# Optimization experiments

Hardware: AMD Instinct MI355X
Metric: run time of the kernel (lower is better)

The kernel has to match this reference:

```python
import jax, jax.numpy as jnp
import numpy as np

B, N, D = 4, 2048, 1024

def setup_inputs() -> dict:
    key = jax.random.key(0)
    ks = jax.random.split(key, 8)
    s = 1.0 / np.sqrt(D)
    return {
        "x": jax.random.normal(ks[0], (B, N, D), dtype=jnp.float32),
        "Wq": jax.random.normal(ks[1], (D, D), dtype=jnp.float32) * s,
        "bq": jnp.zeros((D,), dtype=jnp.float32),
        "Wk": jax.random.normal(ks[2], (D, D), dtype=jnp.float32) * s,
        "bk": jnp.zeros((D,), dtype=jnp.float32),
        "Wv": jax.random.normal(ks[3], (D, D), dtype=jnp.float32) * s,
        "bv": jnp.zeros((D,), dtype=jnp.float32),
        "gamma": jnp.ones((1,), dtype=jnp.float32),
    }

def reference(x, Wq, bq, Wk, bk, Wv, bv, gamma):
    d = x.shape[-1]
    delta = 1.0 / jnp.sqrt(jnp.asarray(d, dtype=x.dtype))
    # torch Linear: y = x @ W.T + b, W is [out, in]
    Q = jnp.einsum('bnd,ed->bne', x, Wq) + bq
    K = jnp.einsum('bnd,ed->bne', x, Wk) + bk
    V = jnp.einsum('bnd,ed->bne', x, Wv) + bv
    scores = jnp.einsum('bne,bme->bnm', Q, K) * delta  # [B, N, N]
    attn = jax.nn.softmax(scores, axis=-1)
    out = jnp.einsum('bnm,bme->bne', attn, V)
    return out * gamma + x
```

## Files before the change

kernel.cpp:

```cpp
#include <hip/hip_runtime.h>

typedef _Float16 f16;
typedef __attribute__((ext_vector_type(4))) _Float16 f16x4;
typedef __attribute__((ext_vector_type(8))) _Float16 f16x8;
typedef __attribute__((ext_vector_type(4))) float f32x4;

#define B_ 4
#define N_ 2048
#define D_ 1024

#define FENCE asm volatile("" ::: "memory")

__global__ __launch_bounds__(256) void k_cast_all(const float4* __restrict__ x,
                                                  const float4* __restrict__ wq,
                                                  const float4* __restrict__ wk,
                                                  const float4* __restrict__ wv,
                                                  f16x4* __restrict__ xo,
                                                  f16x4* __restrict__ wqo,
                                                  f16x4* __restrict__ wko,
                                                  f16x4* __restrict__ wvo,
                                                  float* __restrict__ rowsum) {
  int b = blockIdx.x;
  if (b >= 11264) {
    rowsum[(b - 11264) * 256 + threadIdx.x] = 0.f;
    return;
  }
  const float4* in;
  f16x4* out;
  int idx;
  if (b < 8192)       { in = x;  out = xo;  idx = b * 256 + threadIdx.x; }
  else if (b < 9216)  { in = wq; out = wqo; idx = (b - 8192) * 256 + threadIdx.x; }
  else if (b < 10240) { in = wk; out = wko; idx = (b - 9216) * 256 + threadIdx.x; }
  else                { in = wv; out = wvo; idx = (b - 10240) * 256 + threadIdx.x; }
  float4 v = in[idx];
  f16x4 o = { (_Float16)v.x, (_Float16)v.y, (_Float16)v.z, (_Float16)v.w };
  out[idx] = o;
}

__device__ __forceinline__ void stage_half(const char* g0, int ldB, int kByte,
                                           char* slot, int tid) {
#pragma unroll
  for (int r = 0; r < 2; ++r) {
    int lin = r * 8192 + tid * 16;
    int row = lin >> 7;
    int lch = ((lin >> 4) & 7) ^ (row & 7);
    const char* g = g0 + (long)row * ldB + kByte + lch * 16;
    char* l = slot + r * 8192 + ((tid >> 6) << 10);
    __builtin_amdgcn_global_load_lds(
        (const __attribute__((address_space(1))) unsigned int*)g,
        (__attribute__((address_space(3))) unsigned int*)l, 16, 0, 0);
  }
}

#define RD_A(dst, base)                                                          \
  _Pragma("unroll") for (int i_ = 0; i_ < 4; ++i_) {                             \
    int rA_ = wm * 64 + i_ * 16 + l16;                                           \
    _Pragma("unroll") for (int k_ = 0; k_ < 2; ++k_)                             \
      dst[i_][k_] = *(const f16x8*)((base) + rA_ * 128 +                         \
                                    ((((k_ << 2) | quad) ^ l7) << 4));           \
  }
#define RD_B(dst, base)                                                          \
  _Pragma("unroll") for (int j_ = 0; j_ < 2; ++j_) {                             \
    int rB_ = wn * 32 + j_ * 16 + l16;                                           \
    _Pragma("unroll") for (int k_ = 0; k_ < 2; ++k_)                             \
      dst[j_][k_] = *(const f16x8*)((base) + rB_ * 128 +                         \
                                    ((((k_ << 2) | quad) ^ l7) << 4));           \
  }
#define MFMA8(Av, Bv, BH)                                                        \
  __builtin_amdgcn_s_setprio(1);                                                 \
  _Pragma("unroll") for (int i_ = 0; i_ < 4; ++i_)                               \
  _Pragma("unroll") for (int j_ = 0; j_ < 2; ++j_)                               \
  _Pragma("unroll") for (int k_ = 0; k_ < 2; ++k_)                               \
    acc[i_][BH][j_] = __builtin_amdgcn_mfma_f32_16x16x32_f16(                    \
        Av[i_][k_], Bv[j_][k_], acc[i_][BH][j_], 0, 0, 0);                       \
  __builtin_amdgcn_s_setprio(0);
#define MFMA16(Av, Bv, AH, BH)                                                   \
  __builtin_amdgcn_s_setprio(1);                                                 \
  _Pragma("unroll") for (int i_ = 0; i_ < 4; ++i_)                               \
  _Pragma("unroll") for (int j_ = 0; j_ < 2; ++j_)                               \
  _Pragma("unroll") for (int k_ = 0; k_ < 2; ++k_)                               \
    acc[AH][i_][BH][j_] = __builtin_amdgcn_mfma_f32_16x16x32_f16(                \
        Av[i_][k_], Bv[j_][k_], acc[AH][i_][BH][j_], 0, 0, 0);                   \
  __builtin_amdgcn_s_setprio(0);

__device__ __forceinline__ void gemm256(const char* gA, int ldaB,
                                        const char* gB, int ldbB,
                                        int nK, char* lds, f32x4 acc[2][4][2][2]) {
  const int tid = threadIdx.x;
  const int lane = tid & 63, wave = tid >> 6;
  const int wm = wave >> 2, wn = wave & 3;
  const int quad = lane >> 4, l16 = lane & 15;
  const int l7 = l16 & 7;
  const char* gA1 = gA + (long)128 * ldaB;
  const char* gB1 = gB + (long)128 * ldbB;
  char* Abuf = lds;
  char* Bbuf = lds + 65536;
  f16x8 a0[4][2], a1[4][2], bX[2][2], bY[2][2];
  stage_half(gA,  ldaB, 0, Abuf, tid);
  stage_half(gB,  ldbB, 0, Bbuf, tid);
  stage_half(gA1, ldaB, 0, Abuf + 16384, tid);
  stage_half(gB1, ldbB, 0, Bbuf + 16384, tid);
  asm volatile("s_waitcnt vmcnt(4)" ::: "memory");
  __builtin_amdgcn_s_barrier(); FENCE;
  RD_A(a0, Abuf); RD_B(bX, Bbuf);
  for (int t = 0; t < nK; ++t) {
    const int c = t & 1;
    char* Ac = Abuf + c * 32768;
    char* Bc = Bbuf + c * 32768;
    char* An = Abuf + (c ^ 1) * 32768;
    char* Bn = Bbuf + (c ^ 1) * 32768;
    const bool st = (t + 1 < nK);
    const int kB = (t + 1) << 7;
    if (st) { stage_half(gA, ldaB, kB, An, tid); stage_half(gB, ldbB, kB, Bn, tid); }
    if (st) asm volatile("s_waitcnt vmcnt(6)" ::: "memory");
    else    asm volatile("s_waitcnt vmcnt(2)" ::: "memory");
    __builtin_amdgcn_s_barrier(); FENCE;
    RD_A(a1, Ac + 16384);
    MFMA16(a0, bX, 0, 0);
    if (st) asm volatile("s_waitcnt vmcnt(4)" ::: "memory");
    else    asm volatile("s_waitcnt vmcnt(0)" ::: "memory");
    __builtin_amdgcn_s_barrier(); FENCE;
    RD_B(bY, Bc + 16384);
    MFMA16(a1, bX, 1, 0);
    if (st) { stage_half(gA1, ldaB, kB, An + 16384, tid); stage_half(gB1, ldbB, kB, Bn + 16384, tid); }
    if (st) asm volatile("s_waitcnt vmcnt(4)" ::: "memory");
    __builtin_amdgcn_s_barrier(); FENCE;
    if (st) RD_B(bX, Bn);
    MFMA16(a0, bY, 0, 1);
    __builtin_amdgcn_s_barrier(); FENCE;
    if (st) RD_A(a0, An);
    MFMA16(a1, bY, 1, 1);
  }
  asm volatile("s_waitcnt vmcnt(0)" ::: "memory");
  __builtin_amdgcn_s_barrier();
  FENCE;
}

#define D128_TILE(AC, B0C, AN, B0N, q) {                                         \
  char* Sc = lds + (q) * 49152;                                                  \
  char* Sn = lds + ((q) ^ 1) * 49152;                                            \
  const int kB = (t + 1) << 7;                                                   \
  stage_half(gA, ldaB, kB, Sn, tid);                                             \
  stage_half(gB, ldbB, kB, Sn + 16384, tid);                                     \
  asm volatile("s_waitcnt vmcnt(4)" ::: "memory");                               \
  __builtin_amdgcn_s_barrier(); FENCE;                                           \
  RD_B(b1, Sc + 32768);                                                          \
  MFMA8(AC, B0C, 0);                                                             \
  stage_half(gB1, ldbB, kB, Sn + 32768, tid);                                    \
  asm volatile("s_waitcnt vmcnt(2)" ::: "memory");                               \
  __builtin_amdgcn_s_barrier(); FENCE;                                           \
  RD_A(AN, Sn); RD_B(B0N, Sn + 16384);                                           \
  MFMA8(AC, b1, 1);                                                              \
}
#define D128_TAIL(AC, B0C, q) {                                                  \
  char* Sc = lds + (q) * 49152;                                                  \
  asm volatile("s_waitcnt vmcnt(0)" ::: "memory");                               \
  __builtin_amdgcn_s_barrier(); FENCE;                                           \
  RD_B(b1, Sc + 32768);                                                          \
  MFMA8(AC, B0C, 0);                                                             \
  MFMA8(AC, b1, 1);                                                              \
}

__device__ __forceinline__ void gemm_d128(const char* gA, int ldaB,
                                          const char* gB, int ldbB,
                                          int nK, char* lds, f32x4 acc[4][2][2]) {
  const int tid = threadIdx.x;
  const int lane = tid & 63, wave = tid >> 6;
  const int wm = wave >> 2, wn = wave & 3;
  const int quad = lane >> 4, l16 = lane & 15;
  const int l7 = l16 & 7;
  const char* gB1 = gB + (long)128 * ldbB;
  f16x8 aX[4][2], aY[4][2], b0X[2][2], b0Y[2][2], b1[2][2];
  stage_half(gA,  ldaB, 0, lds, tid);
  stage_half(gB,  ldbB, 0, lds + 16384, tid);
  stage_half(gB1, ldbB, 0, lds + 32768, tid);
  asm volatile("s_waitcnt vmcnt(2)" ::: "memory");
  __builtin_amdgcn_s_barrier(); FENCE;
  RD_A(aX, lds); RD_B(b0X, lds + 16384);
  for (int tb = 0; tb < nK - 2; tb += 2) {
    { const int t = tb;     D128_TILE(aX, b0X, aY, b0Y, 0) }
    { const int t = tb + 1; D128_TILE(aY, b0Y, aX, b0X, 1) }
  }
  { const int t = nK - 2;   D128_TILE(aX, b0X, aY, b0Y, 0) }
  D128_TAIL(aY, b0Y, 1)
  __builtin_amdgcn_s_barrier(); FENCE;
}

__global__ __launch_bounds__(512, 2) void k_qkv(const f16* __restrict__ X,
                                                const f16* __restrict__ Wq,
                                                const f16* __restrict__ Wk,
                                                const f16* __restrict__ Wv,
                                                const float* __restrict__ bq,
                                                const float* __restrict__ bk,
                                                const float* __restrict__ bv,
                                                f16* __restrict__ Q, f16* __restrict__ Ko,
                                                f16* __restrict__ Vt) {
  __shared__ __align__(16) char lds[131072];
  int fid = blockIdx.x;
  int xcd = fid & 7, k = fid >> 3;
  int rowt = xcd * 4 + (k & 3);
  int colt = k >> 2;
  int tm = rowt * 256;
  int w = colt >> 2;
  int tn = (colt & 3) * 256;
  const f16* Wsel = (w == 0) ? Wq : (w == 1) ? Wk : Wv;
  f32x4 acc[2][4][2][2];
#pragma unroll
  for (int Ah = 0; Ah < 2; ++Ah)
#pragma unroll
    for (int i = 0; i < 4; ++i)
#pragma unroll
      for (int Bh = 0; Bh < 2; ++Bh)
#pragma unroll
        for (int jn = 0; jn < 2; ++jn) acc[Ah][i][Bh][jn] = (f32x4){0.f, 0.f, 0.f, 0.f};
  gemm256((const char*)(X + (long)tm * D_), D_ * 2,
          (const char*)(Wsel + (long)tn * D_), D_ * 2, D_ / 64, lds, acc);
  const int tid = threadIdx.x;
  const int lane = tid & 63, wave = tid >> 6;
  const int wm = wave >> 2, wn = wave & 3;
  const int quad = lane >> 4, l16 = lane & 15;
  if (w < 2) {
    const float* bias = w ? bk : bq;
    f16* outp = w ? Ko : Q;
#pragma unroll
    for (int Bh = 0; Bh < 2; ++Bh)
#pragma unroll
      for (int jn = 0; jn < 2; ++jn) {
        int col = tn + Bh * 128 + wn * 32 + jn * 16 + l16;
        float bb = bias[col];
#pragma unroll
        for (int Ah = 0; Ah < 2; ++Ah)
#pragma unroll
          for (int i = 0; i < 4; ++i) {
            int rbase = tm + Ah * 128 + wm * 64 + i * 16 + quad * 4;
#pragma unroll
            for (int r = 0; r < 4; ++r)
              outp[(long)(rbase + r) * D_ + col] = (_Float16)(acc[Ah][i][Bh][jn][r] + bb);
          }
      }
  } else {
    int bidx = tm >> 11, ntok = tm & 2047;
    f16* VtB = Vt + (long)bidx * D_ * N_ + ntok;
    f16* ldsT = (f16*)lds;
#pragma unroll
    for (int pass = 0; pass < 2; ++pass) {
      FENCE;
      __builtin_amdgcn_s_barrier();
      FENCE;
#pragma unroll
      for (int jn = 0; jn < 2; ++jn) {
        int fl = wn * 32 + jn * 16 + l16;
        float bb = bv[tn + pass * 128 + fl];
#pragma unroll
        for (int Ah = 0; Ah < 2; ++Ah)
#pragma unroll
          for (int i = 0; i < 4; ++i) {
            int rl = Ah * 128 + wm * 64 + i * 16 + quad * 4;
            f16x4 p = { (_Float16)(acc[Ah][i][pass][jn][0] + bb),
                        (_Float16)(acc[Ah][i][pass][jn][1] + bb),
                        (_Float16)(acc[Ah][i][pass][jn][2] + bb),
                        (_Float16)(acc[Ah][i][pass][jn][3] + bb) };
            *(f16x4*)(ldsT + fl * 264 + rl) = p;
          }
      }
      FENCE;
      __builtin_amdgcn_s_barrier();
      FENCE;
#pragma unroll
      for (int p = 0; p < 8; ++p) {
        int f = p * 16 + (tid >> 5);
        int cc = tid & 31;
        f16x8 v = *(const f16x8*)(ldsT + f * 264 + cc * 8);
        *(f16x8*)(VtB + (long)(tn + pass * 128 + f) * N_ + cc * 8) = v;
      }
    }
  }
}

__global__ __launch_bounds__(512, 2) void k_scores(const f16* __restrict__ Qf,
                                                   const f16* __restrict__ Kf,
                                                   f16* __restrict__ S,
                                                   float* __restrict__ rowsum) {
  __shared__ __align__(16) char lds[131072];
  int fid = blockIdx.x;
  int xcd = fid & 7, k = fid >> 3;
  int lin = xcd * 32 + k;
  int b = lin >> 6;
  int t = lin & 63;
  int rowt = t & 7, colt = t >> 3;
  int tm = rowt * 256, tn = colt * 256;
  f32x4 acc[2][4][2][2];
#pragma unroll
  for (int Ah = 0; Ah < 2; ++Ah)
#pragma unroll
    for (int i = 0; i < 4; ++i)
#pragma unroll
      for (int Bh = 0; Bh < 2; ++Bh)
#pragma unroll
        for (int jn = 0; jn < 2; ++jn) acc[Ah][i][Bh][jn] = (f32x4){0.f, 0.f, 0.f, 0.f};
  gemm256((const char*)(Qf + (long)b * N_ * D_ + (long)tm * D_), D_ * 2,
          (const char*)(Kf + (long)b * N_ * D_ + (long)tn * D_), D_ * 2,
          D_ / 64, lds, acc);
  const int tid = threadIdx.x;
  const int lane = tid & 63, wave = tid >> 6;
  const int wm = wave >> 2, wn = wave & 3;
  const int quad = lane >> 4, l16 = lane & 15;
  f16* Sb = S + (long)b * N_ * N_;
  const float delta = 0.03125f;
  f16* ldsS = (f16*)lds;
  float rsum[2][4][4];
#pragma unroll
  for (int Ah = 0; Ah < 2; ++Ah)
#pragma unroll
    for (int i = 0; i < 4; ++i)
#pragma unroll
      for (int r = 0; r < 4; ++r) rsum[Ah][i][r] = 0.f;
#pragma unroll
  for (int Bh = 0; Bh < 2; ++Bh) {
    FENCE;
    __builtin_amdgcn_s_barrier();
    FENCE;
#pragma unroll
    for (int Ah = 0; Ah < 2; ++Ah)
#pragma unroll
      for (int i = 0; i < 4; ++i) {
        int rloc = Ah * 128 + wm * 64 + i * 16 + quad * 4;
#pragma unroll
        for (int jn = 0; jn < 2; ++jn) {
          int col = wn * 32 + jn * 16 + l16;
#pragma unroll
          for (int r = 0; r < 4; ++r) {
            float e = __expf(acc[Ah][i][Bh][jn][r] * delta);
            rsum[Ah][i][r] += e;
            ldsS[(rloc + r) * 136 + col] = (_Float16)e;
          }
        }
      }
    FENCE;
    __builtin_amdgcn_s_barrier();
    FENCE;
#pragma unroll
    for (int p = 0; p < 8; ++p) {
      int row = p * 32 + (tid >> 4);
      int cc = tid & 15;
      f16x8 v = *(const f16x8*)(ldsS + row * 136 + cc * 8);
      *(f16x8*)(Sb + (long)(tm + row) * N_ + tn + Bh * 128 + cc * 8) = v;
    }
  }
#pragma unroll
  for (int m = 1; m < 16; m <<= 1)
#pragma unroll
    for (int Ah = 0; Ah < 2; ++Ah)
#pragma unroll
      for (int i = 0; i < 4; ++i)
#pragma unroll
        for (int r = 0; r < 4; ++r) rsum[Ah][i][r] += __shfl_xor(rsum[Ah][i][r], m);
  if (l16 == 0) {
    float* rs = rowsum + (long)b * N_ + tm;
#pragma unroll
    for (int Ah = 0; Ah < 2; ++Ah)
#pragma unroll
      for (int i = 0; i < 4; ++i)
#pragma unroll
        for (int r = 0; r < 4; ++r)
          atomicAdd(rs + Ah * 128 + wm * 64 + i * 16 + quad * 4 + r, rsum[Ah][i][r]);
  }
}

__global__ __launch_bounds__(512, 2) void k_out(const f16* __restrict__ P,
                                                const f16* __restrict__ Vt,
                                                const f16* __restrict__ xf,
                                                const float* __restrict__ gamma,
                                                const float* __restrict__ rowsum,
                                                float* __restrict__ out) {
  __shared__ __align__(16) char lds[98304];
  int fid = blockIdx.x;
  int xcd = fid & 7, kq = fid >> 3;
  int lin = xcd * 32 + kq;
  int b = lin >> 6;
  int t = lin & 63;
  int rowt = t >> 2, colt = t & 3;
  int tm = rowt * 128, tn = colt * 256;
  f32x4 acc[4][2][2];
#pragma unroll
  for (int i = 0; i < 4; ++i)
#pragma unroll
    for (int Bh = 0; Bh < 2; ++Bh)
#pragma unroll
      for (int jn = 0; jn < 2; ++jn) acc[i][Bh][jn] = (f32x4){0.f, 0.f, 0.f, 0.f};
  gemm_d128((const char*)(P + (long)b * N_ * N_ + (long)tm * N_), N_ * 2,
            (const char*)(Vt + (long)b * D_ * N_ + (long)tn * N_), N_ * 2,
            N_ / 64, lds, acc);
  const int tid = threadIdx.x;
  const int lane = tid & 63, wave = tid >> 6;
  const int wm = wave >> 2, wn = wave & 3;
  const int quad = lane >> 4, l16 = lane & 15;
  float g = gamma[0];
  float inv[4][4];
#pragma unroll
  for (int i = 0; i < 4; ++i)
#pragma unroll
    for (int r = 0; r < 4; ++r)
      inv[i][r] = g / rowsum[(long)b * N_ + tm + wm * 64 + i * 16 + quad * 4 + r];
#pragma unroll
  for (int Bh = 0; Bh < 2; ++Bh)
#pragma unroll
    for (int jn = 0; jn < 2; ++jn) {
      int col = tn + Bh * 128 + wn * 32 + jn * 16 + l16;
#pragma unroll
      for (int i = 0; i < 4; ++i) {
        int rbase = tm + wm * 64 + i * 16 + quad * 4;
#pragma unroll
        for (int r = 0; r < 4; ++r) {
          long idx = (long)b * N_ * D_ + (long)(rbase + r) * D_ + col;
          out[idx] = acc[i][Bh][jn][r] * inv[i][r] + (float)xf[idx];
        }
      }
    }
}

extern "C" void kernel_launch(void* const* d_in, const int* in_sizes, int n_in,
                              void* d_out, int out_size, void* d_ws, size_t ws_size,
                              hipStream_t stream) {
  const float* x  = (const float*)d_in[0];
  const float* Wq = (const float*)d_in[1];
  const float* bq = (const float*)d_in[2];
  const float* Wk = (const float*)d_in[3];
  const float* bk = (const float*)d_in[4];
  const float* Wv = (const float*)d_in[5];
  const float* bv = (const float*)d_in[6];
  const float* gamma = (const float*)d_in[7];
  float* out = (float*)d_out;
  char* ws = (char*)d_ws;

  f16* Qb  = (f16*)(ws);
  f16* Kb  = (f16*)(ws + (16u << 20));
  f16* Vt  = (f16*)(ws + (32u << 20));
  f16* Xb  = (f16*)(ws + (48u << 20));
  f16* Wqb = (f16*)(ws + (64u << 20));
  f16* Wkb = (f16*)(ws + (66u << 20));
  f16* Wvb = (f16*)(ws + (68u << 20));
  f16* S   = (f16*)(ws + (64u << 20));
  float* rowsum = (float*)(ws + (96u << 20));

  k_cast_all<<<11296, 256, 0, stream>>>((const float4*)x, (const float4*)Wq,
                                        (const float4*)Wk, (const float4*)Wv,
                                        (f16x4*)Xb, (f16x4*)Wqb, (f16x4*)Wkb, (f16x4*)Wvb,
                                        rowsum);
  k_qkv<<<384, 512, 0, stream>>>(Xb, Wqb, Wkb, Wvb, bq, bk, bv, Qb, Kb, Vt);
  k_scores<<<256, 512, 0, stream>>>(Qb, Kb, S, rowsum);
  k_out<<<256, 512, 0, stream>>>(S, Vt, Xb, gamma, rowsum, out);
}
```

Before: 235.6 us.

## Restructure gemm256 into a two-K-step unrolled pipeline with per-quarter staging

The 256x256 GEMM main loop is unrolled by two K steps, with LDS split into eight named quarter buffers. Each global load is reissued into a quarter buffer as soon as that buffer has been consumed, rather than staging whole halves into an alternate buffer. The prologue prefetches two K steps ahead, keeping about ten loads in flight, and the waitcnts now also drain LDS reads. The schedule assumes nK is even and adds more barriers per iteration; it aims to hide global memory latency more fully.

```diff
diff --git a/kernel.cpp b/kernel.cpp
--- a/kernel.cpp
+++ b/kernel.cpp
@@ -93,47 +93,77 @@
   const int l7 = l16 & 7;
   const char* gA1 = gA + (long)128 * ldaB;
   const char* gB1 = gB + (long)128 * ldbB;
-  char* Abuf = lds;
-  char* Bbuf = lds + 65536;
+  char* const A00 = lds;
+  char* const A10 = lds + 16384;
+  char* const A01 = lds + 32768;
+  char* const A11 = lds + 49152;
+  char* const B00 = lds + 65536;
+  char* const B10 = lds + 81920;
+  char* const B01 = lds + 98304;
+  char* const B11 = lds + 114688;
   f16x8 a0[4][2], a1[4][2], bX[2][2], bY[2][2];
-  stage_half(gA,  ldaB, 0, Abuf, tid);
-  stage_half(gB,  ldbB, 0, Bbuf, tid);
-  stage_half(gA1, ldaB, 0, Abuf + 16384, tid);
-  stage_half(gB1, ldbB, 0, Bbuf + 16384, tid);
-  asm volatile("s_waitcnt vmcnt(4)" ::: "memory");
+  stage_half(gB,  ldbB, 0, B00, tid);
+  stage_half(gA,  ldaB, 0, A00, tid);
+  stage_half(gA1, ldaB, 0, A10, tid);
+  stage_half(gB1, ldbB, 0, B10, tid);
+  stage_half(gB,  ldbB, 128, B01, tid);
+  stage_half(gA1, ldaB, 128, A11, tid);
+  stage_half(gA,  ldaB, 128, A01, tid);
+  stage_half(gB1, ldbB, 128, B11, tid);
+  asm volatile("s_waitcnt vmcnt(12)" ::: "memory");
   __builtin_amdgcn_s_barrier(); FENCE;
-  RD_A(a0, Abuf); RD_B(bX, Bbuf);
-  for (int t = 0; t < nK; ++t) {
-    const int c = t & 1;
-    char* Ac = Abuf + c * 32768;
-    char* Bc = Bbuf + c * 32768;
-    char* An = Abuf + (c ^ 1) * 32768;
-    char* Bn = Bbuf + (c ^ 1) * 32768;
-    const bool st = (t + 1 < nK);
-    const int kB = (t + 1) << 7;
-    if (st) { stage_half(gA, ldaB, kB, An, tid); stage_half(gB, ldbB, kB, Bn, tid); }
-    if (st) asm volatile("s_waitcnt vmcnt(6)" ::: "memory");
-    else    asm volatile("s_waitcnt vmcnt(2)" ::: "memory");
-    __builtin_amdgcn_s_barrier(); FENCE;
-    RD_A(a1, Ac + 16384);
+  RD_B(bX, B00); RD_A(a0, A00);
+  const int nIt = nK >> 1;
+  for (int u = 0; u < nIt; ++u) {
+    const bool st = (u + 1 < nIt);
+    const int kB0 = (u * 2 + 2) << 7;
+    const int kB1 = (u * 2 + 3) << 7;
+    asm volatile("s_waitcnt vmcnt(10) lgkmcnt(0)" ::: "memory");
+    __builtin_amdgcn_s_barrier(); FENCE;
+    if (st) stage_half(gB, ldbB, kB0, B00, tid);
+    RD_A(a1, A10);
     MFMA16(a0, bX, 0, 0);
-    if (st) asm volatile("s_waitcnt vmcnt(4)" ::: "memory");
-    else    asm volatile("s_waitcnt vmcnt(0)" ::: "memory");
-    __builtin_amdgcn_s_barrier(); FENCE;
-    RD_B(bY, Bc + 16384);
+    if (st) asm volatile("s_waitcnt vmcnt(10) lgkmcnt(0)" ::: "memory");
+    else    asm volatile("s_waitcnt vmcnt(8) lgkmcnt(0)" ::: "memory");
+    __builtin_amdgcn_s_barrier(); FENCE;
+    if (st) stage_half(gA, ldaB, kB0, A00, tid);
+    RD_B(bY, B10);
     MFMA16(a1, bX, 1, 0);
-    if (st) { stage_half(gA1, ldaB, kB, An + 16384, tid); stage_half(gB1, ldbB, kB, Bn + 16384, tid); }
-    if (st) asm volatile("s_waitcnt vmcnt(4)" ::: "memory");
-    __builtin_amdgcn_s_barrier(); FENCE;
-    if (st) RD_B(bX, Bn);
+    if (st) asm volatile("s_waitcnt vmcnt(10) lgkmcnt(0)" ::: "memory");
+    else    asm volatile("s_waitcnt vmcnt(6) lgkmcnt(0)" ::: "memory");
+    __builtin_amdgcn_s_barrier(); FENCE;
+    if (st) stage_half(gA1, ldaB, kB0, A10, tid);
+    RD_B(bX, B01);
+    MFMA16(a1, bY, 1, 1);
+    if (st) asm volatile("s_waitcnt vmcnt(10) lgkmcnt(0)" ::: "memory");
+    else    asm volatile("s_waitcnt vmcnt(4) lgkmcnt(0)" ::: "memory");
+    __builtin_amdgcn_s_barrier(); FENCE;
+    if (st) stage_half(gB1, ldbB, kB0, B10, tid);
+    RD_A(a1, A11);
     MFMA16(a0, bY, 0, 1);
-    __builtin_amdgcn_s_barrier(); FENCE;
-    if (st) RD_A(a0, An);
+    if (st) asm volatile("s_waitcnt vmcnt(10) lgkmcnt(0)" ::: "memory");
+    else    asm volatile("s_waitcnt vmcnt(2) lgkmcnt(0)" ::: "memory");
+    __builtin_amdgcn_s_barrier(); FENCE;
+    if (st) stage_half(gB, ldbB, kB1, B01, tid);
+    RD_A(a0, A01);
+    MFMA16(a1, bX, 1, 0);
+    if (st) asm volatile("s_waitcnt vmcnt(10) lgkmcnt(0)" ::: "memory");
+    else    asm volatile("s_waitcnt vmcnt(0) lgkmcnt(0)" ::: "memory");
+    __builtin_amdgcn_s_barrier(); FENCE;
+    if (st) stage_half(gA1, ldaB, kB1, A11, tid);
+    RD_B(bY, B11);
+    MFMA16(a0, bX, 0, 0);
+    if (st) asm volatile("s_waitcnt vmcnt(10) lgkmcnt(0)" ::: "memory");
+    __builtin_amdgcn_s_barrier(); FENCE;
+    if (st) { stage_half(gA, ldaB, kB1, A01, tid); RD_B(bX, B00); }
+    MFMA16(a0, bY, 0, 1);
+    if (st) asm volatile("s_waitcnt vmcnt(10) lgkmcnt(0)" ::: "memory");
+    __builtin_amdgcn_s_barrier(); FENCE;
+    if (st) { stage_half(gB1, ldbB, kB1, B11, tid); RD_A(a0, A00); }
     MFMA16(a1, bY, 1, 1);
   }
-  asm volatile("s_waitcnt vmcnt(0)" ::: "memory");
-  __builtin_amdgcn_s_barrier();
-  FENCE;
+  asm volatile("s_waitcnt vmcnt(0) lgkmcnt(0)" ::: "memory");
+  __builtin_amdgcn_s_barrier(); FENCE;
 }
 
 #define D128_TILE(AC, B0C, AN, B0N, q) {                                         \
```

Result: slower. 346.1 us (+46.9%).

## Use 4-wave 128x128-per-wave GEMM tiles for QKV and scores kernels

Applied to the files above, without the earlier changes.

Replaces the 8-wave 256x256 GEMM core with a 4-wave version where each wave computes a 128x128 sub-tile (8x8 MFMA fragments) and reads more operand reuse per LDS load. Staging becomes a simple double-buffered loop with a full vmcnt(0) wait and one barrier per K-step, dropping the finer interleaved waits. The epilogues are rewritten for the new wave layout, with half the waves idle during each LDS transpose pass. This trades latency hiding and occupancy (256 threads, one block per CU, large register footprint) for fewer LDS reads per MFMA.

```diff
diff --git a/kernel.cpp b/kernel.cpp
--- a/kernel.cpp
+++ b/kernel.cpp
@@ -51,6 +51,20 @@
         (__attribute__((address_space(3))) unsigned int*)l, 16, 0, 0);
   }
 }
+__device__ __forceinline__ void stage_half4(const char* g0, int ldB, int kByte,
+                                            char* slot, int tid) {
+#pragma unroll
+  for (int r = 0; r < 4; ++r) {
+    int lin = r * 4096 + tid * 16;
+    int row = lin >> 7;
+    int lch = ((lin >> 4) & 7) ^ (row & 7);
+    const char* g = g0 + (long)row * ldB + kByte + lch * 16;
+    char* l = slot + r * 4096 + ((tid >> 6) << 10);
+    __builtin_amdgcn_global_load_lds(
+        (const __attribute__((address_space(1))) unsigned int*)g,
+        (__attribute__((address_space(3))) unsigned int*)l, 16, 0, 0);
+  }
+}
 
 #define RD_A(dst, base)                                                          \
   _Pragma("unroll") for (int i_ = 0; i_ < 4; ++i_) {                             \
@@ -74,66 +88,67 @@
     acc[i_][BH][j_] = __builtin_amdgcn_mfma_f32_16x16x32_f16(                    \
         Av[i_][k_], Bv[j_][k_], acc[i_][BH][j_], 0, 0, 0);                       \
   __builtin_amdgcn_s_setprio(0);
-#define MFMA16(Av, Bv, AH, BH)                                                   \
+
+#define RD_A8W(dst, base)                                                        \
+  _Pragma("unroll") for (int i_ = 0; i_ < 8; ++i_)                               \
+  _Pragma("unroll") for (int k_ = 0; k_ < 2; ++k_)                               \
+    dst[i_][k_] = *(const f16x8*)((base) + (i_ * 16 + l16) * 128 +               \
+                                  ((((k_ << 2) | quad) ^ l7) << 4));
+#define RD_B2W(dst, base, jp)                                                    \
+  _Pragma("unroll") for (int jj_ = 0; jj_ < 2; ++jj_)                            \
+  _Pragma("unroll") for (int k_ = 0; k_ < 2; ++k_)                               \
+    dst[(jp) * 2 + jj_][k_] = *(const f16x8*)((base) +                           \
+        (((jp) * 2 + jj_) * 16 + l16) * 128 + ((((k_ << 2) | quad) ^ l7) << 4));
+#define MFMA_P4(Av, Bv, Cc, jp)                                                  \
   __builtin_amdgcn_s_setprio(1);                                                 \
-  _Pragma("unroll") for (int i_ = 0; i_ < 4; ++i_)                               \
-  _Pragma("unroll") for (int j_ = 0; j_ < 2; ++j_)                               \
+  _Pragma("unroll") for (int i_ = 0; i_ < 8; ++i_)                               \
+  _Pragma("unroll") for (int jj_ = 0; jj_ < 2; ++jj_)                            \
   _Pragma("unroll") for (int k_ = 0; k_ < 2; ++k_)                               \
-    acc[AH][i_][BH][j_] = __builtin_amdgcn_mfma_f32_16x16x32_f16(                \
-        Av[i_][k_], Bv[j_][k_], acc[AH][i_][BH][j_], 0, 0, 0);                   \
+    Cc[i_][(jp) * 2 + jj_] = __builtin_amdgcn_mfma_f32_16x16x32_f16(             \
+        Av[i_][k_], Bv[(jp) * 2 + jj_][k_], Cc[i_][(jp) * 2 + jj_], 0, 0, 0);    \
   __builtin_amdgcn_s_setprio(0);
 
-__device__ __forceinline__ void gemm256(const char* gA, int ldaB,
-                                        const char* gB, int ldbB,
-                                        int nK, char* lds, f32x4 acc[2][4][2][2]) {
+__device__ __forceinline__ void gemm4w(const char* gA, int ldaB,
+                                       const char* gB, int ldbB,
+                                       int nK, char* lds, f32x4 acc[8][8]) {
   const int tid = threadIdx.x;
   const int lane = tid & 63, wave = tid >> 6;
-  const int wm = wave >> 2, wn = wave & 3;
+  const int wm = wave >> 1, wn = wave & 1;
   const int quad = lane >> 4, l16 = lane & 15;
   const int l7 = l16 & 7;
   const char* gA1 = gA + (long)128 * ldaB;
   const char* gB1 = gB + (long)128 * ldbB;
-  char* Abuf = lds;
-  char* Bbuf = lds + 65536;
-  f16x8 a0[4][2], a1[4][2], bX[2][2], bY[2][2];
-  stage_half(gA,  ldaB, 0, Abuf, tid);
-  stage_half(gB,  ldbB, 0, Bbuf, tid);
-  stage_half(gA1, ldaB, 0, Abuf + 16384, tid);
-  stage_half(gB1, ldbB, 0, Bbuf + 16384, tid);
-  asm volatile("s_waitcnt vmcnt(4)" ::: "memory");
-  __builtin_amdgcn_s_barrier(); FENCE;
-  RD_A(a0, Abuf); RD_B(bX, Bbuf);
+  f16x8 af[8][2], bf[8][2];
+  stage_half4(gA,  ldaB, 0, lds,         tid);
+  stage_half4(gA1, ldaB, 0, lds + 16384, tid);
+  stage_half4(gB,  ldbB, 0, lds + 32768, tid);
+  stage_half4(gB1, ldbB, 0, lds + 49152, tid);
   for (int t = 0; t < nK; ++t) {
-    const int c = t & 1;
-    char* Ac = Abuf + c * 32768;
-    char* Bc = Bbuf + c * 32768;
-    char* An = Abuf + (c ^ 1) * 32768;
-    char* Bn = Bbuf + (c ^ 1) * 32768;
+    char* buf  = lds + (t & 1) * 65536;
+    char* nbuf = lds + ((t + 1) & 1) * 65536;
+    const char* Ah = buf + wm * 16384;
+    const char* Bh = buf + 32768 + wn * 16384;
     const bool st = (t + 1 < nK);
     const int kB = (t + 1) << 7;
-    if (st) { stage_half(gA, ldaB, kB, An, tid); stage_half(gB, ldbB, kB, Bn, tid); }
-    if (st) asm volatile("s_waitcnt vmcnt(6)" ::: "memory");
-    else    asm volatile("s_waitcnt vmcnt(2)" ::: "memory");
+    asm volatile("s_waitcnt vmcnt(0)" ::: "memory");
     __builtin_amdgcn_s_barrier(); FENCE;
-    RD_A(a1, Ac + 16384);
-    MFMA16(a0, bX, 0, 0);
-    if (st) asm volatile("s_waitcnt vmcnt(4)" ::: "memory");
-    else    asm volatile("s_waitcnt vmcnt(0)" ::: "memory");
-    __builtin_amdgcn_s_barrier(); FENCE;
-    RD_B(bY, Bc + 16384);
-    MFMA16(a1, bX, 1, 0);
-    if (st) { stage_half(gA1, ldaB, kB, An + 16384, tid); stage_half(gB1, ldbB, kB, Bn + 16384, tid); }
-    if (st) asm volatile("s_waitcnt vmcnt(4)" ::: "memory");
-    __builtin_amdgcn_s_barrier(); FENCE;
-    if (st) RD_B(bX, Bn);
-    MFMA16(a0, bY, 0, 1);
-    __builtin_amdgcn_s_barrier(); FENCE;
-    if (st) RD_A(a0, An);
-    MFMA16(a1, bY, 1, 1);
-  }
-  asm volatile("s_waitcnt vmcnt(0)" ::: "memory");
-  __builtin_amdgcn_s_barrier();
-  FENCE;
+    if (st) {
+      stage_half4(gA,  ldaB, kB, nbuf,         tid);
+      stage_half4(gA1, ldaB, kB, nbuf + 16384, tid);
+      stage_half4(gB,  ldbB, kB, nbuf + 32768, tid);
+      stage_half4(gB1, ldbB, kB, nbuf + 49152, tid);
+    }
+    RD_A8W(af, Ah);
+    RD_B2W(bf, Bh, 0);
+    RD_B2W(bf, Bh, 1);
+    MFMA_P4(af, bf, acc, 0);
+    RD_B2W(bf, Bh, 2);
+    MFMA_P4(af, bf, acc, 1);
+    RD_B2W(bf, Bh, 3);
+    MFMA_P4(af, bf, acc, 2);
+    MFMA_P4(af, bf, acc, 3);
+  }
+  __builtin_amdgcn_s_barrier(); FENCE;
 }
 
 #define D128_TILE(AC, B0C, AN, B0N, q) {                                         \
@@ -186,7 +201,7 @@
   __builtin_amdgcn_s_barrier(); FENCE;
 }
 
-__global__ __launch_bounds__(512, 2) void k_qkv(const f16* __restrict__ X,
+__global__ __launch_bounds__(256, 1) void k_qkv(const f16* __restrict__ X,
                                                 const f16* __restrict__ Wq,
                                                 const f16* __restrict__ Wk,
                                                 const f16* __restrict__ Wv,
@@ -204,40 +219,32 @@
   int w = colt >> 2;
   int tn = (colt & 3) * 256;
   const f16* Wsel = (w == 0) ? Wq : (w == 1) ? Wk : Wv;
-  f32x4 acc[2][4][2][2];
-#pragma unroll
-  for (int Ah = 0; Ah < 2; ++Ah)
-#pragma unroll
-    for (int i = 0; i < 4; ++i)
-#pragma unroll
-      for (int Bh = 0; Bh < 2; ++Bh)
-#pragma unroll
-        for (int jn = 0; jn < 2; ++jn) acc[Ah][i][Bh][jn] = (f32x4){0.f, 0.f, 0.f, 0.f};
-  gemm256((const char*)(X + (long)tm * D_), D_ * 2,
-          (const char*)(Wsel + (long)tn * D_), D_ * 2, D_ / 64, lds, acc);
+  f32x4 acc[8][8];
+#pragma unroll
+  for (int i = 0; i < 8; ++i)
+#pragma unroll
+    for (int j = 0; j < 8; ++j) acc[i][j] = (f32x4){0.f, 0.f, 0.f, 0.f};
+  gemm4w((const char*)(X + (long)tm * D_), D_ * 2,
+         (const char*)(Wsel + (long)tn * D_), D_ * 2, D_ / 64, lds, acc);
   const int tid = threadIdx.x;
   const int lane = tid & 63, wave = tid >> 6;
-  const int wm = wave >> 2, wn = wave & 3;
+  const int wm = wave >> 1, wn = wave & 1;
   const int quad = lane >> 4, l16 = lane & 15;
   if (w < 2) {
     const float* bias = w ? bk : bq;
     f16* outp = w ? Ko : Q;
 #pragma unroll
-    for (int Bh = 0; Bh < 2; ++Bh)
-#pragma unroll
-      for (int jn = 0; jn < 2; ++jn) {
-        int col = tn + Bh * 128 + wn * 32 + jn * 16 + l16;
-        float bb = bias[col];
-#pragma unroll
-        for (int Ah = 0; Ah < 2; ++Ah)
-#pragma unroll
-          for (int i = 0; i < 4; ++i) {
-            int rbase = tm + Ah * 128 + wm * 64 + i * 16 + quad * 4;
-#pragma unroll
-            for (int r = 0; r < 4; ++r)
-              outp[(long)(rbase + r) * D_ + col] = (_Float16)(acc[Ah][i][Bh][jn][r] + bb);
-          }
+    for (int j = 0; j < 8; ++j) {
+      int col = tn + wn * 128 + j * 16 + l16;
+      float bb = bias[col];
+#pragma unroll
+      for (int i = 0; i < 8; ++i) {
+        int rbase = tm + wm * 128 + i * 16 + quad * 4;
+#pragma unroll
+        for (int r = 0; r < 4; ++r)
+          outp[(long)(rbase + r) * D_ + col] = (_Float16)(acc[i][j][r] + bb);
       }
+    }
   } else {
     int bidx = tm >> 11, ntok = tm & 2047;
     f16* VtB = Vt + (long)bidx * D_ * N_ + ntok;
@@ -247,28 +254,26 @@
       FENCE;
       __builtin_amdgcn_s_barrier();
       FENCE;
-#pragma unroll
-      for (int jn = 0; jn < 2; ++jn) {
-        int fl = wn * 32 + jn * 16 + l16;
-        float bb = bv[tn + pass * 128 + fl];
-#pragma unroll
-        for (int Ah = 0; Ah < 2; ++Ah)
-#pragma unroll
-          for (int i = 0; i < 4; ++i) {
-            int rl = Ah * 128 + wm * 64 + i * 16 + quad * 4;
-            f16x4 p = { (_Float16)(acc[Ah][i][pass][jn][0] + bb),
-                        (_Float16)(acc[Ah][i][pass][jn][1] + bb),
-                        (_Float16)(acc[Ah][i][pass][jn][2] + bb),
-                        (_Float16)(acc[Ah][i][pass][jn][3] + bb) };
+      if (wn == pass) {
+#pragma unroll
+        for (int j = 0; j < 8; ++j) {
+          int fl = j * 16 + l16;
+          float bb = bv[tn + pass * 128 + fl];
+#pragma unroll
+          for (int i = 0; i < 8; ++i) {
+            int rl = wm * 128 + i * 16 + quad * 4;
+            f16x4 p = { (_Float16)(acc[i][j][0] + bb), (_Float16)(acc[i][j][1] + bb),
+                        (_Float16)(acc[i][j][2] + bb), (_Float16)(acc[i][j][3] + bb) };
             *(f16x4*)(ldsT + fl * 264 + rl) = p;
           }
+        }
       }
       FENCE;
       __builtin_amdgcn_s_barrier();
       FENCE;
 #pragma unroll
-      for (int p = 0; p < 8; ++p) {
-        int f = p * 16 + (tid >> 5);
+      for (int p = 0; p < 16; ++p) {
+        int f = p * 8 + (tid >> 5);
         int cc = tid & 31;
         f16x8 v = *(const f16x8*)(ldsT + f * 264 + cc * 8);
         *(f16x8*)(VtB + (long)(tn + pass * 128 + f) * N_ + cc * 8) = v;
@@ -277,7 +282,7 @@
   }
 }
 
-__global__ __launch_bounds__(512, 2) void k_scores(const f16* __restrict__ Qf,
+__global__ __launch_bounds__(256, 1) void k_scores(const f16* __restrict__ Qf,
                                                    const f16* __restrict__ Kf,
                                                    f16* __restrict__ S,
                                                    float* __restrict__ rowsum) {
@@ -289,81 +294,71 @@
   int t = lin & 63;
   int rowt = t & 7, colt = t >> 3;
   int tm = rowt * 256, tn = colt * 256;
-  f32x4 acc[2][4][2][2];
-#pragma unroll
-  for (int Ah = 0; Ah < 2; ++Ah)
-#pragma unroll
-    for (int i = 0; i < 4; ++i)
-#pragma unroll
-      for (int Bh = 0; Bh < 2; ++Bh)
-#pragma unroll
-        for (int jn = 0; jn < 2; ++jn) acc[Ah][i][Bh][jn] = (f32x4){0.f, 0.f, 0.f, 0.f};
-  gemm256((const char*)(Qf + (long)b * N_ * D_ + (long)tm * D_), D_ * 2,
-          (const char*)(Kf + (long)b * N_ * D_ + (long)tn * D_), D_ * 2,
-          D_ / 64, lds, acc);
+  f32x4 acc[8][8];
+#pragma unroll
+  for (int i = 0; i < 8; ++i)
+#pragma unroll
+    for (int j = 0; j < 8; ++j) acc[i][j] = (f32x4){0.f, 0.f, 0.f, 0.f};
+  gemm4w((const char*)(Qf + (long)b * N_ * D_ + (long)tm * D_), D_ * 2,
+         (const char*)(Kf + (long)b * N_ * D_ + (long)tn * D_), D_ * 2,
+         D_ / 64, lds, acc);
   const int tid = threadIdx.x;
   const int lane = tid & 63, wave = tid >> 6;
-  const int wm = wave >> 2, wn = wave & 3;
+  const int wm = wave >> 1, wn = wave & 1;
   const int quad = lane >> 4, l16 = lane & 15;
   f16* Sb = S + (long)b * N_ * N_;
   const float delta = 0.03125f;
   f16* ldsS = (f16*)lds;
-  float rsum[2][4][4];
-#pragma unroll
-  for (int Ah = 0; Ah < 2; ++Ah)
-#pragma unroll
-    for (int i = 0; i < 4; ++i)
-#pragma unroll
-      for (int r = 0; r < 4; ++r) rsum[Ah][i][r] = 0.f;
-#pragma unroll
-  for (int Bh = 0; Bh < 2; ++Bh) {
+  float rsum[8][4];
+#pragma unroll
+  for (int i = 0; i < 8; ++i)
+#pragma unroll
+    for (int r = 0; r < 4; ++r) rsum[i][r] = 0.f;
+#pragma unroll
+  for (int pass = 0; pass < 2; ++pass) {
     FENCE;
     __builtin_amdgcn_s_barrier();
     FENCE;
-#pragma unroll
-    for (int Ah = 0; Ah < 2; ++Ah)
-#pragma unroll
-      for (int i = 0; i < 4; ++i) {
-        int rloc = Ah * 128 + wm * 64 + i * 16 + quad * 4;
-#pragma unroll
-        for (int jn = 0; jn < 2; ++jn) {
-          int col = wn * 32 + jn * 16 + l16;
+    if (wn == pass) {
+#pragma unroll
+      for (int i = 0; i < 8; ++i) {
+        int rloc = wm * 128 + i * 16 + quad * 4;
+#pragma unroll
+        for (int j = 0; j < 8; ++j) {
+          int col = j * 16 + l16;
 #pragma unroll
           for (int r = 0; r < 4; ++r) {
-            float e = __expf(acc[Ah][i][Bh][jn][r] * delta);
-            rsum[Ah][i][r] += e;
+            float e = __expf(acc[i][j][r] * delta);
+            rsum[i][r] += e;
             ldsS[(rloc + r) * 136 + col] = (_Float16)e;
           }
         }
       }
+    }
     FENCE;
     __builtin_amdgcn_s_barrier();
     FENCE;
 #pragma unroll
-    for (int p = 0; p < 8; ++p) {
-      int row = p * 32 + (tid >> 4);
+    for (int p = 0; p < 16; ++p) {
+      int row = p * 16 + (tid >> 4);
       int cc = tid & 15;
       f16x8 v = *(const f16x8*)(ldsS + row * 136 + cc * 8);
-      *(f16x8*)(Sb + (long)(tm + row) * N_ + tn + Bh * 128 + cc * 8) = v;
+      *(f16x8*)(Sb + (long)(tm + row) * N_ + tn + pass * 128 + cc * 8) = v;
     }
   }
 #pragma unroll
   for (int m = 1; m < 16; m <<= 1)
 #pragma unroll
-    for (int Ah = 0; Ah < 2; ++Ah)
-#pragma unroll
-      for (int i = 0; i < 4; ++i)
-#pragma unroll
-        for (int r = 0; r < 4; ++r) rsum[Ah][i][r] += __shfl_xor(rsum[Ah][i][r], m);
+    for (int i = 0; i < 8; ++i)
+#pragma unroll
+      for (int r = 0; r < 4; ++r) rsum[i][r] += __shfl_xor(rsum[i][r], m);
   if (l16 == 0) {
     float* rs = rowsum + (long)b * N_ + tm;
 #pragma unroll
-    for (int Ah = 0; Ah < 2; ++Ah)
-#pragma unroll
-      for (int i = 0; i < 4; ++i)
-#pragma unroll
-        for (int r = 0; r < 4; ++r)
-          atomicAdd(rs + Ah * 128 + wm * 64 + i * 16 + quad * 4 + r, rsum[Ah][i][r]);
+    for (int i = 0; i < 8; ++i)
+#pragma unroll
+      for (int r = 0; r < 4; ++r)
+        atomicAdd(rs + wm * 128 + i * 16 + quad * 4 + r, rsum[i][r]);
   }
 }
 
@@ -447,7 +442,7 @@
                                         (const float4*)Wk, (const float4*)Wv,
                                         (f16x4*)Xb, (f16x4*)Wqb, (f16x4*)Wkb, (f16x4*)Wvb,
                                         rowsum);
-  k_qkv<<<384, 512, 0, stream>>>(Xb, Wqb, Wkb, Wvb, bq, bk, bv, Qb, Kb, Vt);
-  k_scores<<<256, 512, 0, stream>>>(Qb, Kb, S, rowsum);
+  k_qkv<<<384, 256, 0, stream>>>(Xb, Wqb, Wkb, Wvb, bq, bk, bv, Qb, Kb, Vt);
+  k_scores<<<256, 256, 0, stream>>>(Qb, Kb, S, rowsum);
   k_out<<<256, 512, 0, stream>>>(S, Vt, Xb, gamma, rowsum, out);
 }
```

Result: slower. 251.3 us (+6.7%).
